# Optimization experiments

Hardware: AMD Instinct MI355X
Metric: run time of the kernel (lower is better)

## Reference

```python
import jax, jax.numpy as jnp
import numpy as np

NEG_BIG = -9.0e15  # mask value from original code (-9000000000000000.0)


def setup_inputs() -> dict:
    key = jax.random.key(0)
    k1, k2, k3, k4, k5 = jax.random.split(key, 5)
    B, N, M, D = 32, 1024, 1024, 128
    input1 = jax.random.normal(k1, (B, N, D), dtype=jnp.float32)
    input2 = jax.random.normal(k2, (B, M, D), dtype=jnp.float32)
    adj = jax.random.randint(k3, (B, N, M), 0, 2, dtype=jnp.int32)
    # xavier_normal on (D,1): std = gain*sqrt(2/(fan_in+fan_out)) = 1.414*sqrt(2/(D+1))
    std = 1.414 * np.sqrt(2.0 / (D + 1))
    a1 = jax.random.normal(k4, (D, 1), dtype=jnp.float32) * std
    a2 = jax.random.normal(k5, (D, 1), dtype=jnp.float32) * std
    return {"input1": input1, "input2": input2, "adj": adj, "a1": a1, "a2": a2}


def reference(input1, input2, adj, a1, a2):
    h, g = input1, input2
    # e1: (B,N,1), e2: (B,1,M); broadcast add replaces the repeat() calls
    e1 = jnp.matmul(h, a1)                      # (B,N,1)
    e2 = jnp.matmul(g, a2).transpose(0, 2, 1)   # (B,1,M)
    e = jax.nn.leaky_relu(e1 + e2, negative_slope=0.2)  # (B,N,M)
    attention = jnp.where(adj > 0, e, NEG_BIG)
    attention = jax.nn.softmax(attention, axis=2)
    attention = jnp.where(jnp.isnan(attention), 0.0, attention)
    # per-batch loop in original builds adj_[b,i,j] = adj[b,i,:].sum(); vectorized:
    deg = jnp.sum(adj, axis=2, keepdims=True).astype(attention.dtype)  # (B,N,1)
    attention = attention * deg
    h_prime = jnp.matmul(attention, g)          # (B,N,D)
    return h_prime
```

## Files before the change

### kernel.cpp

```cpp
#include <hip/hip_runtime.h>

#define BB 32
#define NN 1024
#define MM 1024
#define DD 128

typedef __attribute__((ext_vector_type(4))) float f32x4;
typedef __attribute__((ext_vector_type(8))) __bf16 bf16x8;
typedef unsigned short ushort_t;
typedef unsigned int uint_t;

#define L2E 1.44269504f
#define KEXP 9.357623e-14f
#define KEXPINV 1.0686475e13f

__device__ __forceinline__ unsigned f2bf(float x) {
    unsigned u = __builtin_bit_cast(unsigned, x);
    return (u + 0x7fffu + ((u >> 16) & 1u)) >> 16;
}

#define GLOAD16(gp, lp)                                                     \
    __builtin_amdgcn_global_load_lds(                                       \
        (const __attribute__((address_space(1))) unsigned int*)(gp),        \
        (__attribute__((address_space(3))) unsigned int*)(lp), 16, 0, 0)

__global__ __launch_bounds__(256) void prep(
    const float* __restrict__ g, const float* __restrict__ h,
    const float* __restrict__ a1, const float* __restrict__ a2,
    ushort_t* __restrict__ gq, float* __restrict__ e1, float* __restrict__ e2)
{
    __shared__ ushort_t tl[DD][66];
    int b = blockIdx.y, m0 = blockIdx.x * 64, t = threadIdx.x;

    #pragma unroll
    for (int i = 0; i < 8; i++) {
        int idx = i * 256 + t;
        int m = idx >> 5;
        int c4 = (idx & 31) * 4;
        float4 v = *(const float4*)(h + ((size_t)(b * NN + m0 + m)) * DD + c4);
        float4 av = *(const float4*)(a1 + c4);
        float p = v.x * av.x + v.y * av.y + v.z * av.z + v.w * av.w;
        #pragma unroll
        for (int s = 16; s; s >>= 1) p += __shfl_xor(p, s);
        if ((t & 31) == 0) e1[b * NN + m0 + m] = p;
    }
    #pragma unroll
    for (int i = 0; i < 8; i++) {
        int idx = i * 256 + t;
        int m = idx >> 5;
        int c4 = (idx & 31) * 4;
        float4 v = *(const float4*)(g + ((size_t)(b * MM + m0 + m)) * DD + c4);
        tl[c4 + 0][m] = (ushort_t)f2bf(v.x);
        tl[c4 + 1][m] = (ushort_t)f2bf(v.y);
        tl[c4 + 2][m] = (ushort_t)f2bf(v.z);
        tl[c4 + 3][m] = (ushort_t)f2bf(v.w);
        float4 av = *(const float4*)(a2 + c4);
        float p = v.x * av.x + v.y * av.y + v.z * av.z + v.w * av.w;
        #pragma unroll
        for (int s = 16; s; s >>= 1) p += __shfl_xor(p, s);
        if ((t & 31) == 0) e2[b * MM + m0 + m] = p;
    }
    __syncthreads();
    #pragma unroll
    for (int i = 0; i < 4; i++) {
        int idx = i * 256 + t;
        int d = idx >> 3;
        int c = (idx & 7) * 8;
        int4 o;
        o.x = (int)((unsigned)tl[d][c + 0] | ((unsigned)tl[d][c + 1] << 16));
        o.y = (int)((unsigned)tl[d][c + 2] | ((unsigned)tl[d][c + 3] << 16));
        o.z = (int)((unsigned)tl[d][c + 4] | ((unsigned)tl[d][c + 5] << 16));
        o.w = (int)((unsigned)tl[d][c + 6] | ((unsigned)tl[d][c + 7] << 16));
        int mg = m0 + c;
        *(int4*)(gq + (((size_t)((b * 32 + (mg >> 5)) * DD + d)) << 5) + (mg & 31)) = o;
    }
}

__global__ __launch_bounds__(256, 2) void attn_tiled(
    const int* __restrict__ adj, const ushort_t* __restrict__ gq,
    const float* __restrict__ e1, const float* __restrict__ e2,
    float* __restrict__ out)
{
    __shared__ __align__(16) float e2S[MM];
    __shared__ __align__(16) int adjS[4][64 * 32];
    __shared__ __align__(16) ushort_t gqS[4][128 * 32];

    int b = blockIdx.y, n0 = blockIdx.x * 64, t = threadIdx.x;
    int wid = t >> 6, lane = t & 63;
    int rlo = lane & 15, hh = lane >> 4;
    int r = wid * 16 + rlo;
    int r8 = r & 7;

    {
        float4 ev = *(const float4*)(e2 + b * MM + t * 4);
        ev.x *= L2E; ev.y *= L2E; ev.z *= L2E; ev.w *= L2E;
        *(float4*)(&e2S[t * 4]) = ev;
    }
    float e1f = L2E * e1[b * NN + n0 + r];
    __syncthreads();

    const int* adjb = adj + (size_t)(b * NN + n0) * MM;
    const ushort_t* gqb = gq + (size_t)b * (32 * DD * 32);

    int adi0 = t, adi1 = t + 256;
    int arow0 = adi0 >> 3, aseg0 = (adi0 & 7) ^ (arow0 & 7);
    int arow1 = adi1 >> 3, aseg1 = (adi1 & 7) ^ (arow1 & 7);
    int gd0 = adi0 >> 2, gseg0 = (adi0 & 3) ^ ((gd0 >> 1) & 3);
    int gd1 = adi1 >> 2, gseg1 = (adi1 & 3) ^ ((gd1 >> 1) & 3);

#define STAGE(P, K) do {                                                    \
        GLOAD16(adjb + (size_t)arow0 * MM + (K) * 32 + aseg0 * 4,           \
                &adjS[P][adi0 * 4]);                                        \
        GLOAD16(adjb + (size_t)arow1 * MM + (K) * 32 + aseg1 * 4,           \
                &adjS[P][adi1 * 4]);                                        \
        GLOAD16(gqb + (size_t)(K) * 4096 + gd0 * 32 + gseg0 * 8,            \
                &gqS[P][adi0 * 8]);                                         \
        GLOAD16(gqb + (size_t)(K) * 4096 + gd1 * 32 + gseg1 * 8,            \
                &gqS[P][adi1 * 8]);                                         \
    } while (0)

    f32x4 acc[8];
    #pragma unroll
    for (int j = 0; j < 8; j++) acc[j] = (f32x4){0.f, 0.f, 0.f, 0.f};
    float zl = 0.f, dl = 0.f;

#define COMPUTE(P, K) do {                                                  \
        int4 a0 = *(const int4*)(&adjS[P][r * 32 + ((2 * hh) ^ r8) * 4]);   \
        int4 a1 = *(const int4*)(&adjS[P][r * 32 + ((2 * hh + 1) ^ r8) * 4]);\
        float4 ev0 = *(const float4*)(&e2S[(K) * 32 + 8 * hh]);             \
        float4 ev1 = *(const float4*)(&e2S[(K) * 32 + 8 * hh + 4]);         \
        float ex[8] = {ev0.x, ev0.y, ev0.z, ev0.w,                          \
                       ev1.x, ev1.y, ev1.z, ev1.w};                         \
        int   ax[8] = {a0.x, a0.y, a0.z, a0.w, a1.x, a1.y, a1.z, a1.w};     \
        bf16x8 af;                                                          \
        _Pragma("unroll")                                                   \
        for (int jj = 0; jj < 8; jj++) {                                    \
            float sp = e1f + ex[jj];                                        \
            float lk = fmaxf(sp, 0.2f * sp);                                \
            float sel = (ax[jj] > 0) ? KEXP : 0.f;                          \
            float wv = sel * __builtin_amdgcn_exp2f(lk);                    \
            zl += wv;                                                       \
            dl += sel;                                                      \
            af[jj] = (__bf16)wv;                                            \
        }                                                                   \
        _Pragma("unroll")                                                   \
        for (int j = 0; j < 8; j++) {                                       \
            int d = j * 16 + rlo;                                           \
            int4 bv = *(const int4*)(                                       \
                &gqS[P][d * 32 + (hh ^ ((rlo >> 1) & 3)) * 8]);             \
            acc[j] = __builtin_amdgcn_mfma_f32_16x16x32_bf16(               \
                         af, __builtin_bit_cast(bf16x8, bv), acc[j], 0,0,0);\
        }                                                                   \
    } while (0)

    STAGE(0, 0); STAGE(1, 1); STAGE(2, 2);

    for (int k = 0; k < 30; ++k) {
        asm volatile("s_waitcnt vmcnt(8)" ::: "memory");
        __builtin_amdgcn_s_barrier();
        __builtin_amdgcn_sched_barrier(0);
        if (k < 29) STAGE((k + 3) & 3, k + 3);
        COMPUTE(k & 3, k);
    }
    asm volatile("s_waitcnt vmcnt(4)" ::: "memory");
    __builtin_amdgcn_s_barrier();
    __builtin_amdgcn_sched_barrier(0);
    COMPUTE(2, 30);
    asm volatile("s_waitcnt vmcnt(0)" ::: "memory");
    __builtin_amdgcn_s_barrier();
    __builtin_amdgcn_sched_barrier(0);
    COMPUTE(3, 31);

#undef COMPUTE
#undef STAGE

    zl += __shfl_xor(zl, 16); zl += __shfl_xor(zl, 32);
    dl += __shfl_xor(dl, 16); dl += __shfl_xor(dl, 32);
    float sc = (dl > 0.f) ? (dl * KEXPINV) / zl : 0.f;

    float scr[4];
    #pragma unroll
    for (int rg = 0; rg < 4; rg++) scr[rg] = __shfl(sc, 4 * hh + rg);

    float* ob = out + ((size_t)(b * NN + n0 + wid * 16)) * DD + rlo;
    #pragma unroll
    for (int j = 0; j < 8; j++)
        #pragma unroll
        for (int rg = 0; rg < 4; rg++)
            ob[(size_t)(4 * hh + rg) * DD + j * 16] = acc[j][rg] * scr[rg];
}

extern "C" void kernel_launch(void* const* d_in, const int* in_sizes, int n_in,
                              void* d_out, int out_size, void* d_ws, size_t ws_size,
                              hipStream_t stream) {
    const float* h   = (const float*)d_in[0];
    const float* g   = (const float*)d_in[1];
    const int*   adj = (const int*)d_in[2];
    const float* a1  = (const float*)d_in[3];
    const float* a2  = (const float*)d_in[4];
    float* out = (float*)d_out;

    char* ws = (char*)d_ws;
    float*    e1 = (float*)(ws);
    float*    e2 = (float*)(ws + (128u << 10));
    ushort_t* gq = (ushort_t*)(ws + (512u << 10));

    prep<<<dim3(MM / 64, BB), 256, 0, stream>>>(g, h, a1, a2, gq, e1, e2);
    attn_tiled<<<dim3(NN / 64, BB), 256, 0, stream>>>(adj, gq, e1, e2, out);
}
```

Measured before the change: 48.09 us.

## Halve row tile and split D across waves to raise occupancy

Each block now handles 32 rows instead of 64. The four waves are arranged as 2 row-groups × 2 D-halves, and each computes 4 MFMA accumulators instead of 8. The LDS ring shrinks from 4 to 3 stages, and launch bounds allow 4 blocks per CU, giving more concurrent blocks to hide adjacency-stream latency. In exchange, the gq tiles are reloaded twice as often overall, and the exp/softmax weights are computed redundantly by the two D-half waves.

```diff
diff --git a/kernel.cpp b/kernel.cpp
--- a/kernel.cpp
+++ b/kernel.cpp
@@ -76,19 +76,20 @@
     }
 }
 
-__global__ __launch_bounds__(256, 2) void attn_tiled(
+__global__ __launch_bounds__(256, 4) void attn_tiled(
     const int* __restrict__ adj, const ushort_t* __restrict__ gq,
     const float* __restrict__ e1, const float* __restrict__ e2,
     float* __restrict__ out)
 {
     __shared__ __align__(16) float e2S[MM];
-    __shared__ __align__(16) int adjS[4][64 * 32];
-    __shared__ __align__(16) ushort_t gqS[4][128 * 32];
-
-    int b = blockIdx.y, n0 = blockIdx.x * 64, t = threadIdx.x;
+    __shared__ __align__(16) int adjS[3][32 * 32];
+    __shared__ __align__(16) ushort_t gqS[3][128 * 32];
+
+    int b = blockIdx.y, n0 = blockIdx.x * 32, t = threadIdx.x;
     int wid = t >> 6, lane = t & 63;
+    int wr = wid >> 1, wd = wid & 1;
     int rlo = lane & 15, hh = lane >> 4;
-    int r = wid * 16 + rlo;
+    int r = wr * 16 + rlo;
     int r8 = r & 7;
 
     {
@@ -102,26 +103,23 @@
     const int* adjb = adj + (size_t)(b * NN + n0) * MM;
     const ushort_t* gqb = gq + (size_t)b * (32 * DD * 32);
 
-    int adi0 = t, adi1 = t + 256;
-    int arow0 = adi0 >> 3, aseg0 = (adi0 & 7) ^ (arow0 & 7);
-    int arow1 = adi1 >> 3, aseg1 = (adi1 & 7) ^ (arow1 & 7);
-    int gd0 = adi0 >> 2, gseg0 = (adi0 & 3) ^ ((gd0 >> 1) & 3);
-    int gd1 = adi1 >> 2, gseg1 = (adi1 & 3) ^ ((gd1 >> 1) & 3);
+    int arow = t >> 3, aseg = (t & 7) ^ (arow & 7);
+    int di0 = t, di1 = t + 256;
+    int gd0 = di0 >> 2, gseg0 = (di0 & 3) ^ ((gd0 >> 1) & 3);
+    int gd1 = di1 >> 2, gseg1 = (di1 & 3) ^ ((gd1 >> 1) & 3);
 
 #define STAGE(P, K) do {                                                    \
-        GLOAD16(adjb + (size_t)arow0 * MM + (K) * 32 + aseg0 * 4,           \
-                &adjS[P][adi0 * 4]);                                        \
-        GLOAD16(adjb + (size_t)arow1 * MM + (K) * 32 + aseg1 * 4,           \
-                &adjS[P][adi1 * 4]);                                        \
+        GLOAD16(adjb + (size_t)arow * MM + (K) * 32 + aseg * 4,             \
+                &adjS[P][t * 4]);                                           \
         GLOAD16(gqb + (size_t)(K) * 4096 + gd0 * 32 + gseg0 * 8,            \
-                &gqS[P][adi0 * 8]);                                         \
+                &gqS[P][di0 * 8]);                                          \
         GLOAD16(gqb + (size_t)(K) * 4096 + gd1 * 32 + gseg1 * 8,            \
-                &gqS[P][adi1 * 8]);                                         \
+                &gqS[P][di1 * 8]);                                          \
     } while (0)
 
-    f32x4 acc[8];
-    #pragma unroll
-    for (int j = 0; j < 8; j++) acc[j] = (f32x4){0.f, 0.f, 0.f, 0.f};
+    f32x4 acc[4];
+    #pragma unroll
+    for (int j = 0; j < 4; j++) acc[j] = (f32x4){0.f, 0.f, 0.f, 0.f};
     float zl = 0.f, dl = 0.f;
 
 #define COMPUTE(P, K) do {                                                  \
@@ -144,8 +142,8 @@
             af[jj] = (__bf16)wv;                                            \
         }                                                                   \
         _Pragma("unroll")                                                   \
-        for (int j = 0; j < 8; j++) {                                       \
-            int d = j * 16 + rlo;                                           \
+        for (int j = 0; j < 4; j++) {                                       \
+            int d = wd * 64 + j * 16 + rlo;                                 \
             int4 bv = *(const int4*)(                                       \
                 &gqS[P][d * 32 + (hh ^ ((rlo >> 1) & 3)) * 8]);             \
             acc[j] = __builtin_amdgcn_mfma_f32_16x16x32_bf16(               \
@@ -153,23 +151,22 @@
         }                                                                   \
     } while (0)
 
-    STAGE(0, 0); STAGE(1, 1); STAGE(2, 2);
-
-    for (int k = 0; k < 30; ++k) {
-        asm volatile("s_waitcnt vmcnt(8)" ::: "memory");
+    STAGE(0, 0); STAGE(1, 1);
+
+    int pk = 0, p2 = 2;
+    for (int k = 0; k < 31; ++k) {
+        asm volatile("s_waitcnt vmcnt(3)" ::: "memory");
         __builtin_amdgcn_s_barrier();
         __builtin_amdgcn_sched_barrier(0);
-        if (k < 29) STAGE((k + 3) & 3, k + 3);
-        COMPUTE(k & 3, k);
-    }
-    asm volatile("s_waitcnt vmcnt(4)" ::: "memory");
-    __builtin_amdgcn_s_barrier();
-    __builtin_amdgcn_sched_barrier(0);
-    COMPUTE(2, 30);
+        if (k < 30) STAGE(p2, k + 2);
+        COMPUTE(pk, k);
+        pk = (pk == 2) ? 0 : pk + 1;
+        p2 = (p2 == 2) ? 0 : p2 + 1;
+    }
     asm volatile("s_waitcnt vmcnt(0)" ::: "memory");
     __builtin_amdgcn_s_barrier();
     __builtin_amdgcn_sched_barrier(0);
-    COMPUTE(3, 31);
+    COMPUTE(pk, 31);
 
 #undef COMPUTE
 #undef STAGE
@@ -182,9 +179,9 @@
     #pragma unroll
     for (int rg = 0; rg < 4; rg++) scr[rg] = __shfl(sc, 4 * hh + rg);
 
-    float* ob = out + ((size_t)(b * NN + n0 + wid * 16)) * DD + rlo;
-    #pragma unroll
-    for (int j = 0; j < 8; j++)
+    float* ob = out + ((size_t)(b * NN + n0 + wr * 16)) * DD + wd * 64 + rlo;
+    #pragma unroll
+    for (int j = 0; j < 4; j++)
         #pragma unroll
         for (int rg = 0; rg < 4; rg++)
             ob[(size_t)(4 * hh + rg) * DD + j * 16] = acc[j][rg] * scr[rg];
@@ -206,5 +203,5 @@
     ushort_t* gq = (ushort_t*)(ws + (512u << 10));
 
     prep<<<dim3(MM / 64, BB), 256, 0, stream>>>(g, h, a1, a2, gq, e1, e2);
-    attn_tiled<<<dim3(NN / 64, BB), 256, 0, stream>>>(adj, gq, e1, e2, out);
-}
+    attn_tiled<<<dim3(NN / 32, BB), 256, 0, stream>>>(adj, gq, e1, e2, out);
+}
```

Measured after the change: 52.90 us. 1.1x slower.

## Pre-pack adjacency into bitmasks and degrees before the attention kernel

Applied to the files above, without the earlier changes.

A new prep stage streams the int32 adjacency once, packs it into per-row 32-bit bitmasks with an XOR swizzle, and computes row degree and e1 in the same pass. The attention kernel then loads the whole 4 KB-per-block mask tile into LDS up front, so its pipelined loop only stages gq tiles. It also uses the precomputed degree instead of accumulating it. The aim is to take the large adjacency stream out of the MFMA pipeline and cut LDS traffic. The cost is an extra launch-level phase and a small mask write/read round trip through global memory.

```diff
diff --git a/kernel.cpp b/kernel.cpp
--- a/kernel.cpp
+++ b/kernel.cpp
@@ -4,6 +4,8 @@
 #define NN 1024
 #define MM 1024
 #define DD 128
+#define PACK_BLOCKS (BB * NN / 4)
+#define PREP_BLOCKS (BB * (MM / 64))
 
 typedef __attribute__((ext_vector_type(4))) float f32x4;
 typedef __attribute__((ext_vector_type(8))) __bf16 bf16x8;
@@ -12,7 +14,6 @@
 
 #define L2E 1.44269504f
 #define KEXP 9.357623e-14f
-#define KEXPINV 1.0686475e13f
 
 __device__ __forceinline__ unsigned f2bf(float x) {
     unsigned u = __builtin_bit_cast(unsigned, x);
@@ -24,123 +25,142 @@
         (const __attribute__((address_space(1))) unsigned int*)(gp),        \
         (__attribute__((address_space(3))) unsigned int*)(lp), 16, 0, 0)
 
-__global__ __launch_bounds__(256) void prep(
-    const float* __restrict__ g, const float* __restrict__ h,
+__global__ __launch_bounds__(256) void pack_prep(
+    const int* __restrict__ adj, const float* __restrict__ h,
+    const float* __restrict__ g,
     const float* __restrict__ a1, const float* __restrict__ a2,
-    ushort_t* __restrict__ gq, float* __restrict__ e1, float* __restrict__ e2)
+    uint_t* __restrict__ maskw, float* __restrict__ degf,
+    float* __restrict__ e1, ushort_t* __restrict__ gq,
+    float* __restrict__ e2)
 {
     __shared__ ushort_t tl[DD][66];
-    int b = blockIdx.y, m0 = blockIdx.x * 64, t = threadIdx.x;
-
-    #pragma unroll
-    for (int i = 0; i < 8; i++) {
-        int idx = i * 256 + t;
-        int m = idx >> 5;
-        int c4 = (idx & 31) * 4;
-        float4 v = *(const float4*)(h + ((size_t)(b * NN + m0 + m)) * DD + c4);
-        float4 av = *(const float4*)(a1 + c4);
-        float p = v.x * av.x + v.y * av.y + v.z * av.z + v.w * av.w;
-        #pragma unroll
-        for (int s = 16; s; s >>= 1) p += __shfl_xor(p, s);
-        if ((t & 31) == 0) e1[b * NN + m0 + m] = p;
+    int t = threadIdx.x;
+
+    if (blockIdx.x < PACK_BLOCKS) {
+        int wave = (blockIdx.x * 256 + t) >> 6;
+        int lane = t & 63;
+        const int* ap = adj + (size_t)wave * MM + lane * 4;
+        int4 v[4];
+        #pragma unroll
+        for (int r = 0; r < 4; r++) v[r] = *(const int4*)(ap + r * 256);
+        float2 x = *(const float2*)(h + (size_t)wave * DD + lane * 2);
+        float2 a = *(const float2*)(a1 + lane * 2);
+        float p = x.x * a.x + x.y * a.y;
+        int cnt = 0;
+        int sw = 2 * (wave & 15);
+        #pragma unroll
+        for (int r = 0; r < 4; r++) {
+            uint_t nib = (v[r].x > 0 ? 1u : 0u) | (v[r].y > 0 ? 2u : 0u)
+                       | (v[r].z > 0 ? 4u : 0u) | (v[r].w > 0 ? 8u : 0u);
+            cnt += __popc(nib);
+            uint_t val = nib << (4 * (lane & 7));
+            val |= __shfl_xor(val, 1);
+            val |= __shfl_xor(val, 2);
+            val |= __shfl_xor(val, 4);
+            if ((lane & 7) == 0) {
+                int w = r * 8 + (lane >> 3);
+                maskw[(size_t)wave * 32 + (w ^ sw)] = val;
+            }
+        }
+        #pragma unroll
+        for (int s = 32; s; s >>= 1) {
+            cnt += __shfl_xor(cnt, s);
+            p   += __shfl_xor(p, s);
+        }
+        if (lane == 0) { degf[wave] = (float)cnt; e1[wave] = p; }
+    } else {
+        int bx = blockIdx.x - PACK_BLOCKS;
+        int b = bx >> 4, m0 = (bx & 15) * 64;
+        #pragma unroll
+        for (int i = 0; i < 8; i++) {
+            int idx = i * 256 + t;
+            int m = idx >> 5;
+            int c4 = (idx & 31) * 4;
+            float4 v = *(const float4*)(g + ((size_t)(b * MM + m0 + m)) * DD + c4);
+            tl[c4 + 0][m] = (ushort_t)f2bf(v.x);
+            tl[c4 + 1][m] = (ushort_t)f2bf(v.y);
+            tl[c4 + 2][m] = (ushort_t)f2bf(v.z);
+            tl[c4 + 3][m] = (ushort_t)f2bf(v.w);
+            float4 av = *(const float4*)(a2 + c4);
+            float p = v.x * av.x + v.y * av.y + v.z * av.z + v.w * av.w;
+            #pragma unroll
+            for (int s = 16; s; s >>= 1) p += __shfl_xor(p, s);
+            if ((t & 31) == 0) e2[b * MM + m0 + m] = p;
+        }
+        __syncthreads();
+        #pragma unroll
+        for (int i = 0; i < 4; i++) {
+            int idx = i * 256 + t;
+            int d = idx >> 3;
+            int c = (idx & 7) * 8;
+            int4 o;
+            o.x = (int)((unsigned)tl[d][c + 0] | ((unsigned)tl[d][c + 1] << 16));
+            o.y = (int)((unsigned)tl[d][c + 2] | ((unsigned)tl[d][c + 3] << 16));
+            o.z = (int)((unsigned)tl[d][c + 4] | ((unsigned)tl[d][c + 5] << 16));
+            o.w = (int)((unsigned)tl[d][c + 6] | ((unsigned)tl[d][c + 7] << 16));
+            int mg = m0 + c;
+            *(int4*)(gq + (((size_t)((b * 32 + (mg >> 5)) * DD + d)) << 5) + (mg & 31)) = o;
+        }
     }
-    #pragma unroll
-    for (int i = 0; i < 8; i++) {
-        int idx = i * 256 + t;
-        int m = idx >> 5;
-        int c4 = (idx & 31) * 4;
-        float4 v = *(const float4*)(g + ((size_t)(b * MM + m0 + m)) * DD + c4);
-        tl[c4 + 0][m] = (ushort_t)f2bf(v.x);
-        tl[c4 + 1][m] = (ushort_t)f2bf(v.y);
-        tl[c4 + 2][m] = (ushort_t)f2bf(v.z);
-        tl[c4 + 3][m] = (ushort_t)f2bf(v.w);
-        float4 av = *(const float4*)(a2 + c4);
-        float p = v.x * av.x + v.y * av.y + v.z * av.z + v.w * av.w;
-        #pragma unroll
-        for (int s = 16; s; s >>= 1) p += __shfl_xor(p, s);
-        if ((t & 31) == 0) e2[b * MM + m0 + m] = p;
-    }
-    __syncthreads();
-    #pragma unroll
-    for (int i = 0; i < 4; i++) {
-        int idx = i * 256 + t;
-        int d = idx >> 3;
-        int c = (idx & 7) * 8;
-        int4 o;
-        o.x = (int)((unsigned)tl[d][c + 0] | ((unsigned)tl[d][c + 1] << 16));
-        o.y = (int)((unsigned)tl[d][c + 2] | ((unsigned)tl[d][c + 3] << 16));
-        o.z = (int)((unsigned)tl[d][c + 4] | ((unsigned)tl[d][c + 5] << 16));
-        o.w = (int)((unsigned)tl[d][c + 6] | ((unsigned)tl[d][c + 7] << 16));
-        int mg = m0 + c;
-        *(int4*)(gq + (((size_t)((b * 32 + (mg >> 5)) * DD + d)) << 5) + (mg & 31)) = o;
-    }
 }
 
 __global__ __launch_bounds__(256, 2) void attn_tiled(
-    const int* __restrict__ adj, const ushort_t* __restrict__ gq,
-    const float* __restrict__ e1, const float* __restrict__ e2,
-    float* __restrict__ out)
+    const uint_t* __restrict__ maskw, const float* __restrict__ degf,
+    const ushort_t* __restrict__ gq, const float* __restrict__ e1,
+    const float* __restrict__ e2, float* __restrict__ out)
 {
     __shared__ __align__(16) float e2S[MM];
-    __shared__ __align__(16) int adjS[4][64 * 32];
+    __shared__ __align__(16) uint_t maskS[64 * 32];
     __shared__ __align__(16) ushort_t gqS[4][128 * 32];
 
     int b = blockIdx.y, n0 = blockIdx.x * 64, t = threadIdx.x;
     int wid = t >> 6, lane = t & 63;
     int rlo = lane & 15, hh = lane >> 4;
     int r = wid * 16 + rlo;
-    int r8 = r & 7;
-
-    {
-        float4 ev = *(const float4*)(e2 + b * MM + t * 4);
-        ev.x *= L2E; ev.y *= L2E; ev.z *= L2E; ev.w *= L2E;
-        *(float4*)(&e2S[t * 4]) = ev;
-    }
+
+    const uint_t* mb = maskw + (size_t)(b * NN + n0) * 32;
+    GLOAD16(mb + t * 4, &maskS[t * 4]);
+    GLOAD16(mb + (t + 256) * 4, &maskS[(t + 256) * 4]);
+    float4 ev = *(const float4*)(e2 + b * MM + t * 4);
     float e1f = L2E * e1[b * NN + n0 + r];
+    float dgv = degf[b * NN + n0 + r];
+    asm volatile("s_waitcnt vmcnt(0)" ::: "memory");
+    ev.x *= L2E; ev.y *= L2E; ev.z *= L2E; ev.w *= L2E;
+    *(float4*)(&e2S[t * 4]) = ev;
     __syncthreads();
 
-    const int* adjb = adj + (size_t)(b * NN + n0) * MM;
     const ushort_t* gqb = gq + (size_t)b * (32 * DD * 32);
-
-    int adi0 = t, adi1 = t + 256;
-    int arow0 = adi0 >> 3, aseg0 = (adi0 & 7) ^ (arow0 & 7);
-    int arow1 = adi1 >> 3, aseg1 = (adi1 & 7) ^ (arow1 & 7);
-    int gd0 = adi0 >> 2, gseg0 = (adi0 & 3) ^ ((gd0 >> 1) & 3);
-    int gd1 = adi1 >> 2, gseg1 = (adi1 & 3) ^ ((gd1 >> 1) & 3);
+    int di0 = t, di1 = t + 256;
+    int gd0 = di0 >> 2, gseg0 = (di0 & 3) ^ ((gd0 >> 1) & 3);
+    int gd1 = di1 >> 2, gseg1 = (di1 & 3) ^ ((gd1 >> 1) & 3);
 
 #define STAGE(P, K) do {                                                    \
-        GLOAD16(adjb + (size_t)arow0 * MM + (K) * 32 + aseg0 * 4,           \
-                &adjS[P][adi0 * 4]);                                        \
-        GLOAD16(adjb + (size_t)arow1 * MM + (K) * 32 + aseg1 * 4,           \
-                &adjS[P][adi1 * 4]);                                        \
         GLOAD16(gqb + (size_t)(K) * 4096 + gd0 * 32 + gseg0 * 8,            \
-                &gqS[P][adi0 * 8]);                                         \
+                &gqS[P][di0 * 8]);                                          \
         GLOAD16(gqb + (size_t)(K) * 4096 + gd1 * 32 + gseg1 * 8,            \
-                &gqS[P][adi1 * 8]);                                         \
+                &gqS[P][di1 * 8]);                                          \
     } while (0)
 
     f32x4 acc[8];
     #pragma unroll
     for (int j = 0; j < 8; j++) acc[j] = (f32x4){0.f, 0.f, 0.f, 0.f};
-    float zl = 0.f, dl = 0.f;
+    float zl = 0.f;
 
 #define COMPUTE(P, K) do {                                                  \
-        int4 a0 = *(const int4*)(&adjS[P][r * 32 + ((2 * hh) ^ r8) * 4]);   \
-        int4 a1 = *(const int4*)(&adjS[P][r * 32 + ((2 * hh + 1) ^ r8) * 4]);\
+        uint_t mw = maskS[r * 32 + ((K) ^ (2 * rlo))];                      \
+        uint_t mby = (mw >> (8 * hh)) & 0xffu;                              \
         float4 ev0 = *(const float4*)(&e2S[(K) * 32 + 8 * hh]);             \
         float4 ev1 = *(const float4*)(&e2S[(K) * 32 + 8 * hh + 4]);         \
         float ex[8] = {ev0.x, ev0.y, ev0.z, ev0.w,                          \
                        ev1.x, ev1.y, ev1.z, ev1.w};                         \
-        int   ax[8] = {a0.x, a0.y, a0.z, a0.w, a1.x, a1.y, a1.z, a1.w};     \
         bf16x8 af;                                                          \
         _Pragma("unroll")                                                   \
         for (int jj = 0; jj < 8; jj++) {                                    \
             float sp = e1f + ex[jj];                                        \
             float lk = fmaxf(sp, 0.2f * sp);                                \
-            float sel = (ax[jj] > 0) ? KEXP : 0.f;                          \
+            float sel = ((mby >> jj) & 1u) ? KEXP : 0.f;                    \
             float wv = sel * __builtin_amdgcn_exp2f(lk);                    \
             zl += wv;                                                       \
-            dl += sel;                                                      \
             af[jj] = (__bf16)wv;                                            \
         }                                                                   \
         _Pragma("unroll")                                                   \
@@ -156,13 +176,13 @@
     STAGE(0, 0); STAGE(1, 1); STAGE(2, 2);
 
     for (int k = 0; k < 30; ++k) {
-        asm volatile("s_waitcnt vmcnt(8)" ::: "memory");
+        asm volatile("s_waitcnt vmcnt(4)" ::: "memory");
         __builtin_amdgcn_s_barrier();
         __builtin_amdgcn_sched_barrier(0);
         if (k < 29) STAGE((k + 3) & 3, k + 3);
         COMPUTE(k & 3, k);
     }
-    asm volatile("s_waitcnt vmcnt(4)" ::: "memory");
+    asm volatile("s_waitcnt vmcnt(2)" ::: "memory");
     __builtin_amdgcn_s_barrier();
     __builtin_amdgcn_sched_barrier(0);
     COMPUTE(2, 30);
@@ -175,8 +195,7 @@
 #undef STAGE
 
     zl += __shfl_xor(zl, 16); zl += __shfl_xor(zl, 32);
-    dl += __shfl_xor(dl, 16); dl += __shfl_xor(dl, 32);
-    float sc = (dl > 0.f) ? (dl * KEXPINV) / zl : 0.f;
+    float sc = (dgv > 0.f) ? (dgv / zl) : 0.f;
 
     float scr[4];
     #pragma unroll
@@ -201,10 +220,13 @@
     float* out = (float*)d_out;
 
     char* ws = (char*)d_ws;
-    float*    e1 = (float*)(ws);
-    float*    e2 = (float*)(ws + (128u << 10));
-    ushort_t* gq = (ushort_t*)(ws + (512u << 10));
-
-    prep<<<dim3(MM / 64, BB), 256, 0, stream>>>(g, h, a1, a2, gq, e1, e2);
-    attn_tiled<<<dim3(NN / 64, BB), 256, 0, stream>>>(adj, gq, e1, e2, out);
-}
+    float*    e1   = (float*)(ws);
+    float*    e2   = (float*)(ws + (128u << 10));
+    float*    degf = (float*)(ws + (256u << 10));
+    uint_t*   mask = (uint_t*)(ws + (384u << 10));
+    ushort_t* gq   = (ushort_t*)(ws + (384u << 10) + (4u << 20));
+
+    pack_prep<<<dim3(PACK_BLOCKS + PREP_BLOCKS), 256, 0, stream>>>(
+        adj, h, g, a1, a2, mask, degf, e1, gq, e2);
+    attn_tiled<<<dim3(NN / 64, BB), 256, 0, stream>>>(mask, degf, gq, e1, e2, out);
+}
```

After: 58.96 us. +22.6%, slower.

## Factor leaky-relu exponential into per-row and per-column exp products

Applied to the files above, without the earlier changes.

Rewrites exp(leaky_relu(e1+e2)) as a selection between exp(e1)*exp(e2) and exp(0.2e1)*exp(0.2e2). The column factors are precomputed in the prep kernel and the row factors once per thread, so the inner loop needs only a compare, a multiply and a select instead of a transcendental exp per element. This removes the per-element v_exp from the hot loop but adds a second LDS array and extra LDS reads. It also drops the constant-max scaling, which risks float overflow or underflow for large logits, though logits here are small.

```diff
diff --git a/kernel.cpp b/kernel.cpp
--- a/kernel.cpp
+++ b/kernel.cpp
@@ -11,8 +11,6 @@
 typedef unsigned int uint_t;
 
 #define L2E 1.44269504f
-#define KEXP 9.357623e-14f
-#define KEXPINV 1.0686475e13f
 
 __device__ __forceinline__ unsigned f2bf(float x) {
     unsigned u = __builtin_bit_cast(unsigned, x);
@@ -27,7 +25,8 @@
 __global__ __launch_bounds__(256) void prep(
     const float* __restrict__ g, const float* __restrict__ h,
     const float* __restrict__ a1, const float* __restrict__ a2,
-    ushort_t* __restrict__ gq, float* __restrict__ e1, float* __restrict__ e2)
+    ushort_t* __restrict__ gq, float* __restrict__ e1,
+    float* __restrict__ e2B, float* __restrict__ e2D)
 {
     __shared__ ushort_t tl[DD][66];
     int b = blockIdx.y, m0 = blockIdx.x * 64, t = threadIdx.x;
@@ -58,7 +57,10 @@
         float p = v.x * av.x + v.y * av.y + v.z * av.z + v.w * av.w;
         #pragma unroll
         for (int s = 16; s; s >>= 1) p += __shfl_xor(p, s);
-        if ((t & 31) == 0) e2[b * MM + m0 + m] = p;
+        if ((t & 31) == 0) {
+            e2B[b * MM + m0 + m] = __builtin_amdgcn_exp2f(L2E * p);
+            e2D[b * MM + m0 + m] = __builtin_amdgcn_exp2f(0.2f * L2E * p);
+        }
     }
     __syncthreads();
     #pragma unroll
@@ -78,10 +80,11 @@
 
 __global__ __launch_bounds__(256, 2) void attn_tiled(
     const int* __restrict__ adj, const ushort_t* __restrict__ gq,
-    const float* __restrict__ e1, const float* __restrict__ e2,
-    float* __restrict__ out)
+    const float* __restrict__ e1, const float* __restrict__ e2B,
+    const float* __restrict__ e2D, float* __restrict__ out)
 {
-    __shared__ __align__(16) float e2S[MM];
+    __shared__ __align__(16) float BfS[MM];
+    __shared__ __align__(16) float DfS[MM];
     __shared__ __align__(16) int adjS[4][64 * 32];
     __shared__ __align__(16) ushort_t gqS[4][128 * 32];
 
@@ -91,12 +94,12 @@
     int r = wid * 16 + rlo;
     int r8 = r & 7;
 
-    {
-        float4 ev = *(const float4*)(e2 + b * MM + t * 4);
-        ev.x *= L2E; ev.y *= L2E; ev.z *= L2E; ev.w *= L2E;
-        *(float4*)(&e2S[t * 4]) = ev;
-    }
-    float e1f = L2E * e1[b * NN + n0 + r];
+    *(float4*)(&BfS[t * 4]) = *(const float4*)(e2B + b * MM + t * 4);
+    *(float4*)(&DfS[t * 4]) = *(const float4*)(e2D + b * MM + t * 4);
+    float e1r = e1[b * NN + n0 + r];
+    float An   = __builtin_amdgcn_exp2f(L2E * e1r);
+    float Cn   = __builtin_amdgcn_exp2f(0.2f * L2E * e1r);
+    float invA = __builtin_amdgcn_exp2f(-L2E * e1r);
     __syncthreads();
 
     const int* adjb = adj + (size_t)(b * NN + n0) * MM;
@@ -122,25 +125,26 @@
     f32x4 acc[8];
     #pragma unroll
     for (int j = 0; j < 8; j++) acc[j] = (f32x4){0.f, 0.f, 0.f, 0.f};
-    float zl = 0.f, dl = 0.f;
+    float zl = 0.f;
+    int dcnt = 0;
 
 #define COMPUTE(P, K) do {                                                  \
         int4 a0 = *(const int4*)(&adjS[P][r * 32 + ((2 * hh) ^ r8) * 4]);   \
         int4 a1 = *(const int4*)(&adjS[P][r * 32 + ((2 * hh + 1) ^ r8) * 4]);\
-        float4 ev0 = *(const float4*)(&e2S[(K) * 32 + 8 * hh]);             \
-        float4 ev1 = *(const float4*)(&e2S[(K) * 32 + 8 * hh + 4]);         \
-        float ex[8] = {ev0.x, ev0.y, ev0.z, ev0.w,                          \
-                       ev1.x, ev1.y, ev1.z, ev1.w};                         \
+        float4 b0 = *(const float4*)(&BfS[(K) * 32 + 8 * hh]);              \
+        float4 b1 = *(const float4*)(&BfS[(K) * 32 + 8 * hh + 4]);          \
+        float4 d0 = *(const float4*)(&DfS[(K) * 32 + 8 * hh]);              \
+        float4 d1 = *(const float4*)(&DfS[(K) * 32 + 8 * hh + 4]);          \
+        float Bv[8] = {b0.x, b0.y, b0.z, b0.w, b1.x, b1.y, b1.z, b1.w};     \
+        float Dv[8] = {d0.x, d0.y, d0.z, d0.w, d1.x, d1.y, d1.z, d1.w};     \
         int   ax[8] = {a0.x, a0.y, a0.z, a0.w, a1.x, a1.y, a1.z, a1.w};     \
         bf16x8 af;                                                          \
         _Pragma("unroll")                                                   \
         for (int jj = 0; jj < 8; jj++) {                                    \
-            float sp = e1f + ex[jj];                                        \
-            float lk = fmaxf(sp, 0.2f * sp);                                \
-            float sel = (ax[jj] > 0) ? KEXP : 0.f;                          \
-            float wv = sel * __builtin_amdgcn_exp2f(lk);                    \
+            float val = (Bv[jj] > invA) ? Bv[jj] * An : Dv[jj] * Cn;        \
+            float wv = (ax[jj] > 0) ? val : 0.f;                            \
             zl += wv;                                                       \
-            dl += sel;                                                      \
+            dcnt += ax[jj];                                                 \
             af[jj] = (__bf16)wv;                                            \
         }                                                                   \
         _Pragma("unroll")                                                   \
@@ -175,8 +179,8 @@
 #undef STAGE
 
     zl += __shfl_xor(zl, 16); zl += __shfl_xor(zl, 32);
-    dl += __shfl_xor(dl, 16); dl += __shfl_xor(dl, 32);
-    float sc = (dl > 0.f) ? (dl * KEXPINV) / zl : 0.f;
+    dcnt += __shfl_xor(dcnt, 16); dcnt += __shfl_xor(dcnt, 32);
+    float sc = (dcnt > 0) ? ((float)dcnt / zl) : 0.f;
 
     float scr[4];
     #pragma unroll
@@ -201,10 +205,11 @@
     float* out = (float*)d_out;
 
     char* ws = (char*)d_ws;
-    float*    e1 = (float*)(ws);
-    float*    e2 = (float*)(ws + (128u << 10));
-    ushort_t* gq = (ushort_t*)(ws + (512u << 10));
-
-    prep<<<dim3(MM / 64, BB), 256, 0, stream>>>(g, h, a1, a2, gq, e1, e2);
-    attn_tiled<<<dim3(NN / 64, BB), 256, 0, stream>>>(adj, gq, e1, e2, out);
-}
+    float*    e1  = (float*)(ws);
+    float*    e2B = (float*)(ws + (128u << 10));
+    float*    e2D = (float*)(ws + (256u << 10));
+    ushort_t* gq  = (ushort_t*)(ws + (512u << 10));
+
+    prep<<<dim3(MM / 64, BB), 256, 0, stream>>>(g, h, a1, a2, gq, e1, e2B, e2D);
+    attn_tiled<<<dim3(NN / 64, BB), 256, 0, stream>>>(adj, gq, e1, e2B, e2D, out);
+}
```

Measured after the change: 48.15 us. No clear change (+0.1%).
